# Kernel optimization log

Hardware: AMD Instinct MI355X
Metric: run time of the kernel (lower is better)

## Reference

```python
import jax, jax.numpy as jnp
import numpy as np

D = 4096
B = 4096


def build_H(n):
    # Sylvester Hadamard matrix, entries +-1, unnormalized (matches repo's build_H)
    H = jnp.ones((1, 1), jnp.float32)
    base = jnp.array([[1.0, 1.0], [1.0, -1.0]], jnp.float32)
    for _ in range(int(np.log2(n))):
        H = jnp.kron(base, H)
    return H


def fwht(x):
    # Unnormalized fast Walsh-Hadamard transform along the last axis.
    # fwht(v) == H @ v for Sylvester H. x: (..., n), n a power of two.
    shape = x.shape
    n = shape[-1]
    x = x.reshape(-1, n)
    h = 1
    while h < n:
        x = x.reshape(-1, n // (2 * h), 2, h)
        a = x[:, :, 0, :]
        b = x[:, :, 1, :]
        x = jnp.stack([a + b, a - b], axis=2).reshape(-1, n)
        h *= 2
    return x.reshape(shape)


def w_bar(u, s1, s2, H):
    # diag(s1) @ FWHT( diag(u) @ (H * s2) )  ==  diag(s1) H diag(u) H diag(s2)
    M = u[:, None] * (H * s2[None, :])          # (D, D)
    return s1[:, None] * fwht(M.T).T             # FWHT along axis 0 == H @ M


def setup_inputs() -> dict:
    key = jax.random.key(0)
    k0, k1, k2 = jax.random.split(key, 3)
    x = jax.random.normal(k0, (B, D), dtype=jnp.float32)
    epsilon = jax.random.normal(k1, (D,), dtype=jnp.float32)
    s1 = jnp.ones((D,), jnp.float32) * 0.01
    s2 = jnp.ones((D,), jnp.float32) * 0.01
    g_mu = jnp.zeros((D,), jnp.float32)
    g_rho = jax.random.uniform(k2, (D,), jnp.float32, minval=-5.0, maxval=-4.0)
    return {"x": x, "epsilon": epsilon, "s1": s1, "s2": s2, "g_mu": g_mu, "g_rho": g_rho}


def reference(x, epsilon, s1, s2, g_mu, g_rho):
    H = build_H(D)
    sigma = jax.nn.softplus(g_rho)               # g_sigma_sqrt_diagonal
    W = w_bar(g_mu, s1, s2, H) + w_bar(sigma * epsilon, s1, s2, H)  # (D, D)
    return x @ W.T                               # (B, D)
```

## Files before the change

### kernel.cpp

```cpp
#include <hip/hip_runtime.h>
#include <cstddef>

#define DSZ 4096

__global__ void compute_v_kernel(const float* __restrict__ eps,
                                 const float* __restrict__ g_mu,
                                 const float* __restrict__ g_rho,
                                 float* __restrict__ v) {
    int i = blockIdx.x * blockDim.x + threadIdx.x;
    if (i < DSZ) {
        float rho = g_rho[i];
        float sp = fmaxf(rho, 0.0f) + log1pf(expf(-fabsf(rho)));
        v[i] = g_mu[i] + sp * eps[i];
    }
}

#define FWHT64(Y) do {                                                  \
    _Pragma("unroll")                                                   \
    for (int s_ = 1; s_ < 64; s_ <<= 1) {                               \
        _Pragma("unroll")                                               \
        for (int r_ = 0; r_ < 64; ++r_) {                               \
            if ((r_ & s_) == 0) {                                       \
                float a_ = Y[r_];                                       \
                float b_ = Y[r_ | s_];                                  \
                Y[r_]      = a_ + b_;                                   \
                Y[r_ | s_] = a_ - b_;                                   \
            }                                                           \
        }                                                               \
    }                                                                   \
} while (0)

#define EXCHANGE(Y) do {                                                \
    __syncthreads();           \
    _Pragma("unroll")                                                   \
    for (int r_ = 0; r_ < 64; ++r_) {                                   \
        int d_ = r_ * 64 + t;                                           \
        lds[d_ ^ ((r_ & 15) << 2)] = Y[r_];                             \
    }                                                                   \
    __syncthreads();                           \
    _Pragma("unroll")                                                   \
    for (int k_ = 0; k_ < 16; ++k_) {                                   \
        int d_ = t * 64 + k_ * 4;                                       \
        float4 vv_ = *(const float4*)&lds[d_ ^ ((t & 15) << 2)];        \
        Y[4 * k_ + 0] = vv_.x;                                          \
        Y[4 * k_ + 1] = vv_.y;                                          \
        Y[4 * k_ + 2] = vv_.z;                                          \
        Y[4 * k_ + 3] = vv_.w;                                          \
    }                                                                   \
} while (0)

__global__ __launch_bounds__(64, 2) void whvi_kernel(
        const float* __restrict__ x,
        const float* __restrict__ s1,
        const float* __restrict__ s2,
        const float* __restrict__ v,
        float* __restrict__ out) {
    __shared__ float lds[DSZ];
    const int t = threadIdx.x;
    const int b = blockIdx.x;

    const float4* x4  = (const float4*)(x + (size_t)b * DSZ);
    const float4* s24 = (const float4*)s2;
    float y[64];

    #pragma unroll
    for (int k = 0; k < 16; ++k) {
        float4 xv = x4[t * 16 + k];
        float4 sv = s24[t * 16 + k];
        y[4 * k + 0] = xv.x * sv.x;
        y[4 * k + 1] = xv.y * sv.y;
        y[4 * k + 2] = xv.z * sv.z;
        y[4 * k + 3] = xv.w * sv.w;
    }

    FWHT64(y);
    EXCHANGE(y);
    FWHT64(y);

    #pragma unroll
    for (int r = 0; r < 64; ++r) {
        y[r] *= v[r * 64 + t];
    }

    FWHT64(y);
    EXCHANGE(y);
    FWHT64(y);

    const float4* s14 = (const float4*)s1;
    float4* o4 = (float4*)(out + (size_t)b * DSZ);
    #pragma unroll
    for (int k = 0; k < 16; ++k) {
        float4 sv = s14[t * 16 + k];
        float4 ov;
        ov.x = y[4 * k + 0] * sv.x;
        ov.y = y[4 * k + 1] * sv.y;
        ov.z = y[4 * k + 2] * sv.z;
        ov.w = y[4 * k + 3] * sv.w;
        o4[t * 16 + k] = ov;
    }
}

extern "C" void kernel_launch(void* const* d_in, const int* in_sizes, int n_in,
                              void* d_out, int out_size, void* d_ws, size_t ws_size,
                              hipStream_t stream) {
    const float* x     = (const float*)d_in[0];
    const float* eps   = (const float*)d_in[1];
    const float* s1    = (const float*)d_in[2];
    const float* s2    = (const float*)d_in[3];
    const float* g_mu  = (const float*)d_in[4];
    const float* g_rho = (const float*)d_in[5];
    float* out = (float*)d_out;
    float* v   = (float*)d_ws;

    compute_v_kernel<<<DSZ / 256, 256, 0, stream>>>(eps, g_mu, g_rho, v);
    whvi_kernel<<<4096, 64, 0, stream>>>(x, s1, s2, v, out);
}
```

Baseline: 151.0 us.

## Split each row's FWHT across 256 threads with radix-16 stages

Each block now uses 256 threads instead of 64, and each thread holds 16 values instead of 64. The 4096-point transform becomes three radix-16 passes with LDS transposes between them, with a new XOR swizzle on the LDS addresses. Global loads and stores become coalesced across threads, register pressure drops, and occupancy rises. In exchange there are more LDS round trips and barriers per row.

```diff
diff --git a/kernel.cpp b/kernel.cpp
--- a/kernel.cpp
+++ b/kernel.cpp
@@ -15,11 +15,15 @@
     }
 }
 
-#define FWHT64(Y) do {                                                  \
+__device__ __forceinline__ int swz(int a) {
+    return a ^ (((a >> 6) & 15) << 2);
+}
+
+#define FWHT16(Y) do {                                                  \
     _Pragma("unroll")                                                   \
-    for (int s_ = 1; s_ < 64; s_ <<= 1) {                               \
+    for (int s_ = 1; s_ < 16; s_ <<= 1) {                               \
         _Pragma("unroll")                                               \
-        for (int r_ = 0; r_ < 64; ++r_) {                               \
+        for (int r_ = 0; r_ < 16; ++r_) {                               \
             if ((r_ & s_) == 0) {                                       \
                 float a_ = Y[r_];                                       \
                 float b_ = Y[r_ | s_];                                  \
@@ -30,73 +34,96 @@
     }                                                                   \
 } while (0)
 
-#define EXCHANGE(Y) do {                                                \
-    __syncthreads();           \
-    _Pragma("unroll")                                                   \
-    for (int r_ = 0; r_ < 64; ++r_) {                                   \
-        int d_ = r_ * 64 + t;                                           \
-        lds[d_ ^ ((r_ & 15) << 2)] = Y[r_];                             \
-    }                                                                   \
-    __syncthreads();                           \
-    _Pragma("unroll")                                                   \
-    for (int k_ = 0; k_ < 16; ++k_) {                                   \
-        int d_ = t * 64 + k_ * 4;                                       \
-        float4 vv_ = *(const float4*)&lds[d_ ^ ((t & 15) << 2)];        \
-        Y[4 * k_ + 0] = vv_.x;                                          \
-        Y[4 * k_ + 1] = vv_.y;                                          \
-        Y[4 * k_ + 2] = vv_.z;                                          \
-        Y[4 * k_ + 3] = vv_.w;                                          \
-    }                                                                   \
-} while (0)
-
-__global__ __launch_bounds__(64, 2) void whvi_kernel(
+__global__ __launch_bounds__(256, 8) void whvi_kernel(
         const float* __restrict__ x,
         const float* __restrict__ s1,
         const float* __restrict__ s2,
         const float* __restrict__ v,
         float* __restrict__ out) {
     __shared__ float lds[DSZ];
-    const int t = threadIdx.x;
+    const int T = threadIdx.x;
     const int b = blockIdx.x;
+    float y[16];
 
     const float4* x4  = (const float4*)(x + (size_t)b * DSZ);
     const float4* s24 = (const float4*)s2;
-    float y[64];
+    #pragma unroll
+    for (int j = 0; j < 4; ++j) {
+        float4 xv = x4[T + 256 * j];
+        float4 sv = s24[T + 256 * j];
+        y[4 * j + 0] = xv.x * sv.x;
+        y[4 * j + 1] = xv.y * sv.y;
+        y[4 * j + 2] = xv.z * sv.z;
+        y[4 * j + 3] = xv.w * sv.w;
+    }
+
+    FWHT16(y);
 
     #pragma unroll
-    for (int k = 0; k < 16; ++k) {
-        float4 xv = x4[t * 16 + k];
-        float4 sv = s24[t * 16 + k];
-        y[4 * k + 0] = xv.x * sv.x;
-        y[4 * k + 1] = xv.y * sv.y;
-        y[4 * k + 2] = xv.z * sv.z;
-        y[4 * k + 3] = xv.w * sv.w;
+    for (int j = 0; j < 4; ++j) {
+        *(float4*)&lds[swz(4 * T + 1024 * j)] =
+            make_float4(y[4 * j], y[4 * j + 1], y[4 * j + 2], y[4 * j + 3]);
+    }
+    __syncthreads();
+    #pragma unroll
+    for (int r = 0; r < 16; ++r)
+        y[r] = lds[swz((T & 3) + 4 * r + 64 * (T >> 2))];
+
+    FWHT16(y);
+
+    #pragma unroll
+    for (int r = 0; r < 16; ++r)
+        lds[swz((T & 3) + 4 * r + 64 * (T >> 2))] = y[r];
+    __syncthreads();
+    #pragma unroll
+    for (int r = 0; r < 16; ++r)
+        y[r] = lds[swz((T & 63) + 64 * r + 1024 * (T >> 6))];
+
+    FWHT16(y);
+
+    const float* vb = v + (T & 63) + 1024 * (T >> 6);
+    #pragma unroll
+    for (int r = 0; r < 16; ++r)
+        y[r] *= vb[64 * r];
+
+    FWHT16(y);
+
+    #pragma unroll
+    for (int r = 0; r < 16; ++r)
+        lds[swz((T & 63) + 64 * r + 1024 * (T >> 6))] = y[r];
+    __syncthreads();
+    #pragma unroll
+    for (int r = 0; r < 16; ++r)
+        y[r] = lds[swz((T & 3) + 4 * r + 64 * (T >> 2))];
+
+    FWHT16(y);
+
+    #pragma unroll
+    for (int r = 0; r < 16; ++r)
+        lds[swz((T & 3) + 4 * r + 64 * (T >> 2))] = y[r];
+    __syncthreads();
+    #pragma unroll
+    for (int j = 0; j < 4; ++j) {
+        float4 t4 = *(const float4*)&lds[swz(4 * T + 1024 * j)];
+        y[4 * j + 0] = t4.x;
+        y[4 * j + 1] = t4.y;
+        y[4 * j + 2] = t4.z;
+        y[4 * j + 3] = t4.w;
     }
 
-    FWHT64(y);
-    EXCHANGE(y);
-    FWHT64(y);
-
-    #pragma unroll
-    for (int r = 0; r < 64; ++r) {
-        y[r] *= v[r * 64 + t];
-    }
-
-    FWHT64(y);
-    EXCHANGE(y);
-    FWHT64(y);
+    FWHT16(y);
 
     const float4* s14 = (const float4*)s1;
     float4* o4 = (float4*)(out + (size_t)b * DSZ);
     #pragma unroll
-    for (int k = 0; k < 16; ++k) {
-        float4 sv = s14[t * 16 + k];
+    for (int j = 0; j < 4; ++j) {
+        float4 sv = s14[T + 256 * j];
         float4 ov;
-        ov.x = y[4 * k + 0] * sv.x;
-        ov.y = y[4 * k + 1] * sv.y;
-        ov.z = y[4 * k + 2] * sv.z;
-        ov.w = y[4 * k + 3] * sv.w;
-        o4[t * 16 + k] = ov;
+        ov.x = y[4 * j + 0] * sv.x;
+        ov.y = y[4 * j + 1] * sv.y;
+        ov.z = y[4 * j + 2] * sv.z;
+        ov.w = y[4 * j + 3] * sv.w;
+        o4[T + 256 * j] = ov;
     }
 }
 
@@ -113,5 +140,5 @@
     float* v   = (float*)d_ws;
 
     compute_v_kernel<<<DSZ / 256, 256, 0, stream>>>(eps, g_mu, g_rho, v);
-    whvi_kernel<<<4096, 64, 0, stream>>>(x, s1, s2, v, out);
+    whvi_kernel<<<4096, 256, 0, stream>>>(x, s1, s2, v, out);
 }
```

Result: faster. 129.1 us (-14.5%).

## Restructure FWHT kernel: coalesced strided loads, per-wave LDS transpose, permuted v

Applied to the files above, without the earlier changes.

Switches to 256-thread blocks where each wave handles two rows and owns a private 4096-float LDS slice. Blocks now sync with wave barriers instead of __syncthreads. Loads become coalesced: thread t reads float4 chunks t+64k, and the FWHT element order is remapped through a swizzled LDS exchange. The scale vector v is precomputed in permuted order, so each thread reads it as contiguous float4s. Outputs use nontemporal stores. The cost is 64KB of LDS per block, which may limit occupancy.

```diff
diff --git a/kernel.cpp b/kernel.cpp
--- a/kernel.cpp
+++ b/kernel.cpp
@@ -3,16 +3,26 @@
 
 #define DSZ 4096
 
-__global__ void compute_v_kernel(const float* __restrict__ eps,
-                                 const float* __restrict__ g_mu,
-                                 const float* __restrict__ g_rho,
-                                 float* __restrict__ v) {
-    int i = blockIdx.x * blockDim.x + threadIdx.x;
-    if (i < DSZ) {
+__global__ void compute_vperm_kernel(const float* __restrict__ eps,
+                                     const float* __restrict__ g_mu,
+                                     const float* __restrict__ g_rho,
+                                     float* __restrict__ vp) {
+    int p = blockIdx.x * blockDim.x + threadIdx.x;
+    if (p < DSZ) {
+        int t = p >> 6, r = p & 63;
+        int i = (t & 3) + 4 * r + 256 * ((t >> 2) & 3) + 1024 * (t >> 4);
         float rho = g_rho[i];
         float sp = fmaxf(rho, 0.0f) + log1pf(expf(-fabsf(rho)));
-        v[i] = g_mu[i] + sp * eps[i];
+        vp[p] = g_mu[i] + sp * eps[i];
     }
+}
+
+typedef float fv4 __attribute__((ext_vector_type(4)));
+__device__ __forceinline__ void nt_store4(float* dst, float a, float b,
+                                          float c, float d) {
+    fv4 t;
+    t.x = a; t.y = b; t.z = c; t.w = d;
+    __builtin_nontemporal_store(t, (fv4*)dst);
 }
 
 #define FWHT64(Y) do {                                                  \
@@ -30,73 +40,90 @@
     }                                                                   \
 } while (0)
 
-#define EXCHANGE(Y) do {                                                \
-    __syncthreads();           \
-    _Pragma("unroll")                                                   \
-    for (int r_ = 0; r_ < 64; ++r_) {                                   \
-        int d_ = r_ * 64 + t;                                           \
-        lds[d_ ^ ((r_ & 15) << 2)] = Y[r_];                             \
-    }                                                                   \
-    __syncthreads();                           \
-    _Pragma("unroll")                                                   \
-    for (int k_ = 0; k_ < 16; ++k_) {                                   \
-        int d_ = t * 64 + k_ * 4;                                       \
-        float4 vv_ = *(const float4*)&lds[d_ ^ ((t & 15) << 2)];        \
-        Y[4 * k_ + 0] = vv_.x;                                          \
-        Y[4 * k_ + 1] = vv_.y;                                          \
-        Y[4 * k_ + 2] = vv_.z;                                          \
-        Y[4 * k_ + 3] = vv_.w;                                          \
-    }                                                                   \
-} while (0)
-
-__global__ __launch_bounds__(64, 2) void whvi_kernel(
+__global__ __launch_bounds__(256, 2) void whvi_kernel(
         const float* __restrict__ x,
         const float* __restrict__ s1,
         const float* __restrict__ s2,
-        const float* __restrict__ v,
+        const float* __restrict__ vp,
         float* __restrict__ out) {
-    __shared__ float lds[DSZ];
-    const int t = threadIdx.x;
-    const int b = blockIdx.x;
+    __shared__ float lds[4 * DSZ];
+    const int T  = threadIdx.x;
+    const int t  = T & 63;
+    const int w  = T >> 6;
+    float* lds_w = lds + w * DSZ;
 
-    const float4* x4  = (const float4*)(x + (size_t)b * DSZ);
+    const int gw = blockIdx.x * 4 + w;
+    const int Bsw = (t & 3) + 260 * ((t >> 2) & 3) + 1040 * (t >> 4);
+
     const float4* s24 = (const float4*)s2;
+    const float4* s14 = (const float4*)s1;
+    const float4* vp4 = (const float4*)(vp + (size_t)t * 64);
+
     float y[64];
 
-    #pragma unroll
-    for (int k = 0; k < 16; ++k) {
-        float4 xv = x4[t * 16 + k];
-        float4 sv = s24[t * 16 + k];
-        y[4 * k + 0] = xv.x * sv.x;
-        y[4 * k + 1] = xv.y * sv.y;
-        y[4 * k + 2] = xv.z * sv.z;
-        y[4 * k + 3] = xv.w * sv.w;
-    }
+    #pragma unroll 1
+    for (int rr = 0; rr < 2; ++rr) {
+        const size_t row = (size_t)gw * 2 + rr;
+        const float4* x4 = (const float4*)(x + row * DSZ);
 
-    FWHT64(y);
-    EXCHANGE(y);
-    FWHT64(y);
+        #pragma unroll
+        for (int k = 0; k < 16; ++k) {
+            float4 xv = x4[t + 64 * k];
+            float4 sv = s24[t + 64 * k];
+            y[4 * k + 0] = xv.x * sv.x;
+            y[4 * k + 1] = xv.y * sv.y;
+            y[4 * k + 2] = xv.z * sv.z;
+            y[4 * k + 3] = xv.w * sv.w;
+        }
 
-    #pragma unroll
-    for (int r = 0; r < 64; ++r) {
-        y[r] *= v[r * 64 + t];
-    }
+        FWHT64(y);
 
-    FWHT64(y);
-    EXCHANGE(y);
-    FWHT64(y);
+        #pragma unroll
+        for (int k = 0; k < 16; ++k)
+            *(float4*)&lds_w[((4 * t) ^ (4 * k)) + 256 * k] =
+                make_float4(y[4 * k], y[4 * k + 1], y[4 * k + 2], y[4 * k + 3]);
+        __builtin_amdgcn_wave_barrier();
+        #pragma unroll
+        for (int r = 0; r < 64; ++r)
+            y[r] = lds_w[Bsw ^ (4 * r)];
 
-    const float4* s14 = (const float4*)s1;
-    float4* o4 = (float4*)(out + (size_t)b * DSZ);
-    #pragma unroll
-    for (int k = 0; k < 16; ++k) {
-        float4 sv = s14[t * 16 + k];
-        float4 ov;
-        ov.x = y[4 * k + 0] * sv.x;
-        ov.y = y[4 * k + 1] * sv.y;
-        ov.z = y[4 * k + 2] * sv.z;
-        ov.w = y[4 * k + 3] * sv.w;
-        o4[t * 16 + k] = ov;
+        FWHT64(y);
+
+        #pragma unroll
+        for (int m = 0; m < 16; ++m) {
+            float4 vq = vp4[m];
+            y[4 * m + 0] *= vq.x;
+            y[4 * m + 1] *= vq.y;
+            y[4 * m + 2] *= vq.z;
+            y[4 * m + 3] *= vq.w;
+        }
+
+        FWHT64(y);
+
+        #pragma unroll
+        for (int r = 0; r < 64; ++r)
+            lds_w[Bsw ^ (4 * r)] = y[r];
+        __builtin_amdgcn_wave_barrier();
+        #pragma unroll
+        for (int k = 0; k < 16; ++k) {
+            float4 q = *(const float4*)&lds_w[((4 * t) ^ (4 * k)) + 256 * k];
+            y[4 * k + 0] = q.x;
+            y[4 * k + 1] = q.y;
+            y[4 * k + 2] = q.z;
+            y[4 * k + 3] = q.w;
+        }
+
+        FWHT64(y);
+
+        float* outrow = out + row * DSZ;
+        #pragma unroll
+        for (int k = 0; k < 16; ++k) {
+            float4 sv = s14[t + 64 * k];
+            nt_store4(outrow + 4 * (t + 64 * k),
+                      y[4 * k + 0] * sv.x, y[4 * k + 1] * sv.y,
+                      y[4 * k + 2] * sv.z, y[4 * k + 3] * sv.w);
+        }
+        __builtin_amdgcn_wave_barrier();
     }
 }
 
@@ -110,8 +137,8 @@
     const float* g_mu  = (const float*)d_in[4];
     const float* g_rho = (const float*)d_in[5];
     float* out = (float*)d_out;
-    float* v   = (float*)d_ws;
+    float* vp  = (float*)d_ws;
 
-    compute_v_kernel<<<DSZ / 256, 256, 0, stream>>>(eps, g_mu, g_rho, v);
-    whvi_kernel<<<4096, 64, 0, stream>>>(x, s1, s2, v, out);
+    compute_vperm_kernel<<<DSZ / 256, 256, 0, stream>>>(eps, g_mu, g_rho, vp);
+    whvi_kernel<<<DSZ / 8, 256, 0, stream>>>(x, s1, s2, vp, out);
 }
```

Result: slower. 252.5 us (+67.3%).
